# Kernel optimization log

Hardware: AMD Instinct MI355X
Metric: run time of the kernel (lower is better)

The kernel has to match this reference:

```python
import jax, jax.numpy as jnp
import numpy as np

# Module hyperparameters (BNMorph.__init__ defaults + KITTI resolution)
B, H, W = 8, 320, 1024
SEARCH_W = 7      # serachWidth
SEARCH_H = 3      # searchHeight
SPARSITY_RAD = 2
SENSE_R = 20
PIX_DW = 24.0     # pixel_distance_weight
ALPHA_DW = 0.7    # alpha_distance_weight
PIX_MUL_DW = 1.9  # pixel_mulline_distance_weight
ALPHA_PAD = 1.6   # alpha_padding
EDGE_DENSITY = 0.02


def _make_offsets():
    # Exactly mirrors BNMorph.__init__ buffer construction.
    rs = np.arange(-SEARCH_W, SEARCH_W + 1)
    cs = np.arange(-SEARCH_H, SEARCH_H + 1)
    xx, yy = np.meshgrid(rs, cs)
    xx = xx.flatten(); yy = yy.flatten()
    idx = np.argsort(xx ** 2 + yy ** 2)
    xx = xx[idx]; yy = yy[idx]
    ss = np.arange(-SPARSITY_RAD, SPARSITY_RAD + 1)
    sxx, syy = np.meshgrid(ss, ss)
    sxx = sxx.flatten(); syy = syy.flatten()
    cspan = np.arange(-SENSE_R, SENSE_R + 1)
    cxx, cyy = np.meshgrid(cspan, cspan)
    cxx = cxx.flatten(); cyy = cyy.flatten()
    ci = np.argsort(cxx ** 2 + cyy ** 2)
    cxx = cxx[ci]; cyy = cyy[ci]
    f32 = lambda a: jnp.asarray(a, dtype=jnp.float32)
    return f32(xx), f32(yy), f32(sxx), f32(syy), f32(cxx), f32(cyy)


def setup_inputs() -> dict:
    key = jax.random.key(0)
    k1, k2 = jax.random.split(key)
    binMapsrc = (jax.random.uniform(k1, (B, 1, H, W)) < EDGE_DENSITY).astype(jnp.float32)
    binMapdst = (jax.random.uniform(k2, (B, 1, H, W)) < EDGE_DENSITY).astype(jnp.float32)
    xx, yy, sxx, syy, cxx, cyy = _make_offsets()
    return {"binMapsrc": binMapsrc, "binMapdst": binMapdst,
            "xx": xx, "yy": yy, "sxx": sxx, "syy": syy, "cxx": cxx, "cyy": cyy}


def _forward(binMapsrc, binMapdst, xx, yy, sxx, syy, cxx, cyy):
    src = binMapsrc[:, 0] > 0.5  # [B,H,W] bool
    dst = binMapdst[:, 0] > 0.5
    b, h, w = src.shape

    # ---- 1. sparsity filtering of src edge points ----
    # keep an active pixel iff no active pixel precedes it (raster order)
    # inside the sparsity window -> approximates greedy sparsification.
    sdx = sxx.astype(jnp.int32); sdy = syy.astype(jnp.int32)
    prec = ((sdy < 0) | ((sdy == 0) & (sdx < 0))).astype(jnp.float32)
    Ps = jnp.pad(src.astype(jnp.float32),
                 ((0, 0), (SPARSITY_RAD, SPARSITY_RAD), (SPARSITY_RAD, SPARSITY_RAD)))

    def sp_step(acc, off):
        dx, dy, wk = off
        sl = jax.lax.dynamic_slice(Ps, (0, SPARSITY_RAD + dy, SPARSITY_RAD + dx), (b, h, w))
        return acc + sl * wk, None

    acc, _ = jax.lax.scan(sp_step, jnp.zeros((b, h, w), jnp.float32), (sdx, sdy, prec))
    kept = src & (acc < 0.5)

    # ---- 2. windowed nearest-correspondence search in dst ----
    # offsets (xx,yy) are pre-sorted by distance, so the first hit is nearest.
    qdx = xx.astype(jnp.int32); qdy = yy.astype(jnp.int32)
    Pd = jnp.pad(dst, ((0, 0), (SEARCH_H, SEARCH_H), (SEARCH_W, SEARCH_W)))

    def m_step(carry, off):
        found, vx, vy = carry
        dx, dy, dxf, dyf = off
        sl = jax.lax.dynamic_slice(Pd, (0, SEARCH_H + dy, SEARCH_W + dx), (b, h, w))
        hit = sl & kept & (~found)
        vx = jnp.where(hit, dxf, vx)
        vy = jnp.where(hit, dyf, vy)
        return (found | hit, vx, vy), None

    init = (jnp.zeros((b, h, w), bool),
            jnp.zeros((b, h, w), jnp.float32),
            jnp.zeros((b, h, w), jnp.float32))
    (found, vx, vy), _ = jax.lax.scan(m_step, init, (qdx, qdy, xx, yy))

    # ---- 3. distance-weighted morph field (splat = depthwise conv) ----
    d = jnp.sqrt(cxx ** 2 + cyy ** 2)
    wts = ALPHA_DW * jnp.exp(-d * PIX_MUL_DW / PIX_DW)
    R = SENSE_R
    K = jnp.zeros((2 * R + 1, 2 * R + 1), jnp.float32)
    K = K.at[cyy.astype(jnp.int32) + R, cxx.astype(jnp.int32) + R].set(wts)

    m = found.astype(jnp.float32)
    inp = jnp.stack([m, m * vx, m * vy], axis=1)        # [B,3,H,W]
    ker = jnp.tile(K[None, None], (3, 1, 1, 1))          # [3,1,41,41]
    out = jax.lax.conv_general_dilated(
        inp, ker, (1, 1), ((R, R), (R, R)),
        dimension_numbers=("NCHW", "OIHW", "NCHW"), feature_group_count=3)
    den = out[:, 0] + ALPHA_PAD
    dispx = out[:, 1] / den
    dispy = out[:, 2] / den

    ygrid, xgrid = jnp.meshgrid(jnp.arange(h, dtype=jnp.float32),
                                jnp.arange(w, dtype=jnp.float32), indexing="ij")
    morphedx = xgrid + dispx
    morphedy = ygrid + dispy
    orgpts_x = xgrid * m
    orgpts_y = ygrid * m
    correspts_x = (xgrid + vx) * m
    correspts_y = (ygrid + vy) * m
    return morphedx, morphedy, orgpts_x, orgpts_y, correspts_x, correspts_y


def reference(binMapsrc, binMapdst, xx, yy, sxx, syy, cxx, cyy):
    return _forward(binMapsrc, binMapdst, xx, yy, sxx, syy, cxx, cyy)
```

## Files before the change

kernel.cpp:

```cpp
#include <hip/hip_runtime.h>


#define BB 8
#define HH 320
#define WW 1024
#define N_PIX (BB*HH*WW)
#define WPI (HH*(WW/32))
#define RR 20
#define TLW 64
#define TLH 16
#define TXN (WW/TLW)
#define TYN (HH/TLH)
#define NQ 105
#define CAP 160
#define NCR (TLH+40)
#define NSR (NCR+2)
#define NDR (NCR+6)
#define WSTRIDE 53
#define WTABN 2228
#define WTAB_OFF (2*BB*WPI*4)

typedef unsigned long long u64;
typedef float v2f __attribute__((ext_vector_type(2)));

__global__ __launch_bounds__(256) void pack_zero(
    const float* __restrict__ src, const float* __restrict__ dst,
    unsigned* __restrict__ packed, float* __restrict__ wtab_g)
{
    int t = threadIdx.x;
    int i = blockIdx.x * 256 + t;
    if (i < WTABN) {
        int row = i / WSTRIDE, c = i - row * WSTRIDE;
        float v = 0.0f;
        if (row <= 40 && c >= 4 && c <= 44) {
            int dxv = c - 24, dyv = row - 20;
            float d = sqrtf((float)(dxv * dxv + dyv * dyv));
            v = 0.7f * expf((-d * 1.9f) / 24.0f);
        }
        wtab_g[i] = v;
    }
    const float4* p = (i < (N_PIX >> 2)) ? (const float4*)src + i
                                         : (const float4*)dst + (i - (N_PIX >> 2));
    float4 v = *p;
    unsigned nib = (v.x > 0.5f ? 1u : 0u) | (v.y > 0.5f ? 2u : 0u)
                 | (v.z > 0.5f ? 4u : 0u) | (v.w > 0.5f ? 8u : 0u);
    unsigned val = nib << ((t & 7) * 4);
    val |= __shfl_xor(val, 1);
    val |= __shfl_xor(val, 2);
    val |= __shfl_xor(val, 4);
    if ((t & 7) == 0) packed[i >> 3] = val;
}

__global__ __launch_bounds__(128, 5) void fused_morph(
    const unsigned* __restrict__ packed,
    const float* __restrict__ xx, const float* __restrict__ yy,
    const float* __restrict__ wtab_g,
    float* __restrict__ out)
{
    __shared__ __align__(16) float wtab[WTABN];
    __shared__ unsigned sSrc[NSR][6];
    __shared__ unsigned sDst[NDR][6];
    __shared__ __align__(16) unsigned sPt[CAP];
    __shared__ __align__(16) unsigned sWav[2][CAP + 4];
    __shared__ int prank[NQ];
    __shared__ unsigned char sVB[TLH * TLW];
    __shared__ int lcnt;

    int t = threadIdx.x;
    int txT = blockIdx.x, tyT = blockIdx.y, b = blockIdx.z;
    int tx0 = txT * TLW, ty0 = tyT * TLH;
    int wb0 = (tx0 >> 5) - 1;
    const unsigned* psrc = packed + (size_t)b * WPI;
    const unsigned* pdst = packed + (size_t)(BB + b) * WPI;

    for (int i = t; i < WTABN / 4; i += 128)
        ((float4*)wtab)[i] = ((const float4*)wtab_g)[i];
    for (int i = t; i < NSR * 4; i += 128) {
        int r = i >> 2, w = (i & 3) + 1;
        int gy = ty0 - 22 + r, gw = wb0 + (w - 1);
        sSrc[r][w] = (gy >= 0 && gy < HH && gw >= 0 && gw < 32) ? psrc[(gy << 5) + gw] : 0u;
    }
    for (int i = t; i < NDR * 4; i += 128) {
        int r = i >> 2, w = (i & 3) + 1;
        int gy = ty0 - 23 + r, gw = wb0 + (w - 1);
        sDst[r][w] = (gy >= 0 && gy < HH && gw >= 0 && gw < 32) ? pdst[(gy << 5) + gw] : 0u;
    }
    if (t < NDR) { sDst[t][0] = 0; sDst[t][5] = 0; if (t < NSR) { sSrc[t][0] = 0; sSrc[t][5] = 0; } }
    if (t < NQ) {
        int dx = (int)xx[t], dy = (int)yy[t];
        prank[(dy + 3) * 15 + (dx + 7)] = (t << 8) | ((dx + 7) << 4) | (dy + 3);
    }
    ((unsigned*)sVB)[t] = 0; ((unsigned*)sVB)[t + 128] = 0;
    if (t == 0) lcnt = 0;
    __syncthreads();

    for (int task = t; task < NCR * 4; task += 128) {
        int cr = task >> 2, w = (task & 3) + 1;
        unsigned C = sSrc[cr + 2][w];
        unsigned found = 0;
        if (C) {
            #define EXT5(row) ( (u64)((row)[w-1] >> 30) \
                              | ((u64)(row)[w] << 2) \
                              | ((u64)((row)[w+1] & 3u) << 34) )
            u64 a = EXT5(sSrc[cr]) | EXT5(sSrc[cr + 1]);
            u64 or5 = a | (a >> 1) | (a >> 2) | (a >> 3) | (a >> 4);
            u64 e2 = EXT5(sSrc[cr + 2]);
            unsigned kept = C & ~(unsigned)(or5 | e2 | (e2 >> 1));
            if (kept) {
                u64 dil = 0;
                #pragma unroll
                for (int rr = 0; rr < 7; ++rr) {
                    const unsigned* row = sDst[cr + rr];
                    dil |= (u64)(row[w-1] >> 25) | ((u64)row[w] << 7)
                         | ((u64)(row[w+1] & 0x7Fu) << 39);
                }
                u64 a2 = dil | (dil >> 1);
                u64 b2 = a2 | (a2 >> 2);
                u64 c2 = b2 | (b2 >> 4);
                u64 o15 = c2 | (c2 >> 7);
                found = kept & (unsigned)o15;
            }
        }
        if (w == 1) found &= 0xFFFFF000u;
        if (w == 4) found &= 0x000FFFFFu;
        if (found) {
            int nf = __popc(found);
            int base = atomicAdd(&lcnt, nf);
            unsigned fi = found;
            while (fi) {
                int bit = __builtin_ctz(fi); fi &= fi - 1;
                int px = tx0 - 32 + ((w - 1) << 5) + bit;
                if (base < CAP) sPt[base] = (unsigned)((cr << 10) | px);
                ++base;
            }
        }
    }
    __syncthreads();
    int nPts = lcnt; if (nPts > CAP) nPts = CAP;

    for (int i = t; i < nPts; i += 128) {
        unsigned e = sPt[i];
        int cr = (int)(e >> 10), px = (int)(e & 1023u);
        int q = px - tx0 + 25;
        int widx = 1 + (q >> 5), sh = q & 31;
        u64 lo = 0, hi = 0;
        #pragma unroll
        for (int rr = 0; rr < 7; ++rr) {
            const unsigned* row = sDst[cr + rr];
            u64 win = (((u64)row[widx] | ((u64)row[widx + 1] << 32)) >> sh) & 0x7FFFull;
            if (rr < 4) lo |= win << (15 * rr);
            else        hi |= win << (15 * (rr - 4));
        }
        int minv = 0x7FFFFFFF;
        while (lo) { int bb2 = __builtin_ctzll(lo); lo &= lo - 1; int rv = prank[bb2];      if (rv < minv) minv = rv; }
        while (hi) { int bb2 = __builtin_ctzll(hi); hi &= hi - 1; int rv = prank[60 + bb2]; if (rv < minv) minv = rv; }
        int vxp7 = (minv >> 4) & 15, vyp3 = minv & 15;
        int py = ty0 - 20 + cr;
        sPt[i] = (unsigned)px | ((unsigned)py << 10)
               | ((unsigned)vxp7 << 19) | ((unsigned)vyp3 << 23);
        if (px >= tx0 && px < tx0 + TLW && cr >= 20 && cr < 20 + TLH)
            sVB[(cr - 20) * TLW + (px - tx0)] =
                (unsigned char)(0x80 | vxp7 | (vyp3 << 4));
    }
    __syncthreads();

    int lane = t & 63, w = __builtin_amdgcn_readfirstlane(t >> 6);
    int wy0 = ty0 + w * 8;
    int cw = 0;
    for (int base = 0; base < nPts; base += 64) {
        int i = base + lane;
        unsigned pk = (i < nPts) ? sPt[i] : 0xFFFFFFFFu;
        int py = (int)((pk >> 10) & 511u);
        bool pass = (i < nPts) & (py >= wy0 - 20) & (py <= wy0 + 27);
        u64 m = __ballot(pass);
        if (pass) {
            int idx = __popcll(m & ((1ull << lane) - 1ull));
            sWav[w][cw + idx] = pk;
        }
        cw += __popcll(m);
    }
    int c4 = (cw + 3) & ~3;
    if (lane < c4 - cw) sWav[w][cw + lane] = 0xFFFFFFFFu;

    int x0q = tx0 + (t & 15) * 4;
    int y0t = ty0 + (t >> 4) * 2;

    v2f a0p[2][2] = {};
    v2f av[2][4]  = {};

    for (int p = 0; p < c4; p += 4) {
        uint4 P = *(const uint4*)&sWav[w][p];
        #pragma unroll
        for (int k = 0; k < 4; ++k) {
            int spk = __builtin_amdgcn_readfirstlane(
                (int)(k == 0 ? P.x : k == 1 ? P.y : k == 2 ? P.z : P.w));
            int pxp21 = (spk & 1023) + 21;
            int pyp20 = ((spk >> 10) & 511) + 20;
            float pvx = (float)(((spk >> 19) & 15) - 7);
            float pvy = (float)(((spk >> 23) & 7) - 3);
            v2f vv = {pvx, pvy};

            int coff = pxp21 - x0q;
            coff = coff < 0 ? 0 : (coff > 45 ? 45 : coff);
            #pragma unroll
            for (int ry = 0; ry < 2; ++ry) {
                int dyr = pyp20 - (y0t + ry);
                int rowi = ((unsigned)dyr > 40u) ? 41 : dyr;
                const float* wr = &wtab[rowi * WSTRIDE + coff];
                float w3 = wr[0], w2 = wr[1], w1 = wr[2], w0 = wr[3];
                a0p[ry][0] += (v2f){w0, w1};
                a0p[ry][1] += (v2f){w2, w3};
                av[ry][0] += w0 * vv;
                av[ry][1] += w1 * vv;
                av[ry][2] += w2 * vv;
                av[ry][3] += w3 * vv;
            }
        }
    }

    size_t bbase = (size_t)b * HH * WW;
    int lx = x0q - tx0;
    #pragma unroll
    for (int ry = 0; ry < 2; ++ry) {
        int y = y0t + ry;
        int ly = y - ty0;
        unsigned vb4 = *(const unsigned*)&sVB[ly * TLW + lx];
        size_t idx = bbase + (size_t)y * WW + x0q;
        float d0 = a0p[ry][0].x + 1.6f, d1 = a0p[ry][0].y + 1.6f;
        float d2 = a0p[ry][1].x + 1.6f, d3 = a0p[ry][1].y + 1.6f;
        float4 ox = { (float)x0q     + av[ry][0].x / d0, (float)(x0q+1) + av[ry][1].x / d1,
                      (float)(x0q+2) + av[ry][2].x / d2, (float)(x0q+3) + av[ry][3].x / d3 };
        float4 oy = { (float)y + av[ry][0].y / d0, (float)y + av[ry][1].y / d1,
                      (float)y + av[ry][2].y / d2, (float)y + av[ry][3].y / d3 };
        float4 o2, o3, o4, o5;
        float* po2 = &o2.x; float* po3 = &o3.x; float* po4 = &o4.x; float* po5 = &o5.x;
        #pragma unroll
        for (int jj = 0; jj < 4; ++jj) {
            unsigned by = (vb4 >> (8 * jj)) & 255u;
            float fm  = (float)(by >> 7);
            float fvx = (float)((int)(by & 15u) - 7);
            float fvy = (float)((int)((by >> 4) & 7u) - 3);
            float fx  = (float)(x0q + jj);
            po2[jj] = fx * fm;
            po3[jj] = (float)y * fm;
            po4[jj] = (fx + fvx) * fm;
            po5[jj] = ((float)y + fvy) * fm;
        }
        *reinterpret_cast<float4*>(out + idx)                     = ox;
        *reinterpret_cast<float4*>(out + (size_t)N_PIX + idx)     = oy;
        *reinterpret_cast<float4*>(out + 2 * (size_t)N_PIX + idx) = o2;
        *reinterpret_cast<float4*>(out + 3 * (size_t)N_PIX + idx) = o3;
        *reinterpret_cast<float4*>(out + 4 * (size_t)N_PIX + idx) = o4;
        *reinterpret_cast<float4*>(out + 5 * (size_t)N_PIX + idx) = o5;
    }
}

extern "C" void kernel_launch(void* const* d_in, const int* in_sizes, int n_in,
                              void* d_out, int out_size, void* d_ws, size_t ws_size,
                              hipStream_t stream) {
    const float* src = (const float*)d_in[0];
    const float* dst = (const float*)d_in[1];
    const float* xx  = (const float*)d_in[2];
    const float* yy  = (const float*)d_in[3];
    float* out = (float*)d_out;

    unsigned* packed = (unsigned*)d_ws;
    float*    wtab_g = (float*)((char*)d_ws + WTAB_OFF);

    pack_zero<<<(2 * N_PIX / 4) / 256, 256, 0, stream>>>(src, dst, packed, wtab_g);

    dim3 g2(TXN, TYN, BB);
    fused_morph<<<g2, 128, 0, stream>>>(packed, xx, yy, wtab_g, out);
}
```

Baseline: 124.7 us.

## Transpose weight table and remap threads to one column by eight rows

The 41x41 distance-weight table is now stored column-major in shared memory with an odd row stride. Each lane owns one x column and accumulates eight consecutive rows, reading eight contiguous weights per edge point. Previously each thread handled a 4x2 pixel patch, so lanes read table addresses four floats apart; the new layout is meant to cut LDS bank conflicts and simplify index math. In exchange, output stores become scalar per lane rather than float4, and the occupancy hint drops from 5 to 4 blocks.

```diff
diff --git a/kernel.cpp b/kernel.cpp
--- a/kernel.cpp
+++ b/kernel.cpp
@@ -16,8 +16,9 @@
 #define NCR (TLH+40)
 #define NSR (NCR+2)
 #define NDR (NCR+6)
-#define WSTRIDE 53
-#define WTABN 2228
+#define NROWT 55
+#define NCOLT 46
+#define WTABTN 2536
 #define WTAB_OFF (2*BB*WPI*4)
 
 typedef unsigned long long u64;
@@ -29,11 +30,12 @@
 {
     int t = threadIdx.x;
     int i = blockIdx.x * 256 + t;
-    if (i < WTABN) {
-        int row = i / WSTRIDE, c = i - row * WSTRIDE;
+    if (i < WTABTN) {
+        int col = i / NROWT, r = i - col * NROWT;
+        int dyr = r - 7;
         float v = 0.0f;
-        if (row <= 40 && c >= 4 && c <= 44) {
-            int dxv = c - 24, dyv = row - 20;
+        if (col <= 44 && dyr >= 0 && dyr <= 40) {
+            int dxv = col - 20, dyv = dyr - 20;
             float d = sqrtf((float)(dxv * dxv + dyv * dyv));
             v = 0.7f * expf((-d * 1.9f) / 24.0f);
         }
@@ -51,13 +53,13 @@
     if ((t & 7) == 0) packed[i >> 3] = val;
 }
 
-__global__ __launch_bounds__(128, 5) void fused_morph(
+__global__ __launch_bounds__(128, 4) void fused_morph(
     const unsigned* __restrict__ packed,
     const float* __restrict__ xx, const float* __restrict__ yy,
     const float* __restrict__ wtab_g,
     float* __restrict__ out)
 {
-    __shared__ __align__(16) float wtab[WTABN];
+    __shared__ __align__(16) float wtabT[WTABTN];
     __shared__ unsigned sSrc[NSR][6];
     __shared__ unsigned sDst[NDR][6];
     __shared__ __align__(16) unsigned sPt[CAP];
@@ -73,8 +75,8 @@
     const unsigned* psrc = packed + (size_t)b * WPI;
     const unsigned* pdst = packed + (size_t)(BB + b) * WPI;
 
-    for (int i = t; i < WTABN / 4; i += 128)
-        ((float4*)wtab)[i] = ((const float4*)wtab_g)[i];
+    for (int i = t; i < WTABTN / 4; i += 128)
+        ((float4*)wtabT)[i] = ((const float4*)wtab_g)[i];
     for (int i = t; i < NSR * 4; i += 128) {
         int r = i >> 2, w = (i & 3) + 1;
         int gy = ty0 - 22 + r, gw = wb0 + (w - 1);
@@ -182,11 +184,10 @@
     int c4 = (cw + 3) & ~3;
     if (lane < c4 - cw) sWav[w][cw + lane] = 0xFFFFFFFFu;
 
-    int x0q = tx0 + (t & 15) * 4;
-    int y0t = ty0 + (t >> 4) * 2;
-
-    v2f a0p[2][2] = {};
-    v2f av[2][4]  = {};
+    int x = tx0 + lane;
+
+    v2f a0p[4] = {};
+    v2f av[8]  = {};
 
     for (int p = 0; p < c4; p += 4) {
         uint4 P = *(const uint4*)&sWav[w][p];
@@ -194,64 +195,49 @@
         for (int k = 0; k < 4; ++k) {
             int spk = __builtin_amdgcn_readfirstlane(
                 (int)(k == 0 ? P.x : k == 1 ? P.y : k == 2 ? P.z : P.w));
-            int pxp21 = (spk & 1023) + 21;
-            int pyp20 = ((spk >> 10) & 511) + 20;
+            int px = spk & 1023;
+            int q = ((spk >> 10) & 511) + 20 - wy0;
+            q = q < 0 ? 0 : (q > 47 ? 47 : q);
             float pvx = (float)(((spk >> 19) & 15) - 7);
             float pvy = (float)(((spk >> 23) & 7) - 3);
             v2f vv = {pvx, pvy};
 
-            int coff = pxp21 - x0q;
-            coff = coff < 0 ? 0 : (coff > 45 ? 45 : coff);
-            #pragma unroll
-            for (int ry = 0; ry < 2; ++ry) {
-                int dyr = pyp20 - (y0t + ry);
-                int rowi = ((unsigned)dyr > 40u) ? 41 : dyr;
-                const float* wr = &wtab[rowi * WSTRIDE + coff];
-                float w3 = wr[0], w2 = wr[1], w1 = wr[2], w0 = wr[3];
-                a0p[ry][0] += (v2f){w0, w1};
-                a0p[ry][1] += (v2f){w2, w3};
-                av[ry][0] += w0 * vv;
-                av[ry][1] += w1 * vv;
-                av[ry][2] += w2 * vv;
-                av[ry][3] += w3 * vv;
-            }
+            int col = px + 20 - x;
+            col = ((unsigned)col > 40u) ? 45 : col;
+            const float* cb = &wtabT[col * NROWT + q];
+            float w0 = cb[0], w1 = cb[1], w2 = cb[2], w3 = cb[3];
+            float w4 = cb[4], w5 = cb[5], w6 = cb[6], w7 = cb[7];
+            a0p[0] += (v2f){w0, w1};
+            a0p[1] += (v2f){w2, w3};
+            a0p[2] += (v2f){w4, w5};
+            a0p[3] += (v2f){w6, w7};
+            av[7] += w0 * vv;  av[6] += w1 * vv;
+            av[5] += w2 * vv;  av[4] += w3 * vv;
+            av[3] += w4 * vv;  av[2] += w5 * vv;
+            av[1] += w6 * vv;  av[0] += w7 * vv;
         }
     }
 
     size_t bbase = (size_t)b * HH * WW;
-    int lx = x0q - tx0;
+    float fx = (float)x;
     #pragma unroll
-    for (int ry = 0; ry < 2; ++ry) {
-        int y = y0t + ry;
-        int ly = y - ty0;
-        unsigned vb4 = *(const unsigned*)&sVB[ly * TLW + lx];
-        size_t idx = bbase + (size_t)y * WW + x0q;
-        float d0 = a0p[ry][0].x + 1.6f, d1 = a0p[ry][0].y + 1.6f;
-        float d2 = a0p[ry][1].x + 1.6f, d3 = a0p[ry][1].y + 1.6f;
-        float4 ox = { (float)x0q     + av[ry][0].x / d0, (float)(x0q+1) + av[ry][1].x / d1,
-                      (float)(x0q+2) + av[ry][2].x / d2, (float)(x0q+3) + av[ry][3].x / d3 };
-        float4 oy = { (float)y + av[ry][0].y / d0, (float)y + av[ry][1].y / d1,
-                      (float)y + av[ry][2].y / d2, (float)y + av[ry][3].y / d3 };
-        float4 o2, o3, o4, o5;
-        float* po2 = &o2.x; float* po3 = &o3.x; float* po4 = &o4.x; float* po5 = &o5.x;
-        #pragma unroll
-        for (int jj = 0; jj < 4; ++jj) {
-            unsigned by = (vb4 >> (8 * jj)) & 255u;
-            float fm  = (float)(by >> 7);
-            float fvx = (float)((int)(by & 15u) - 7);
-            float fvy = (float)((int)((by >> 4) & 7u) - 3);
-            float fx  = (float)(x0q + jj);
-            po2[jj] = fx * fm;
-            po3[jj] = (float)y * fm;
-            po4[jj] = (fx + fvx) * fm;
-            po5[jj] = ((float)y + fvy) * fm;
-        }
-        *reinterpret_cast<float4*>(out + idx)                     = ox;
-        *reinterpret_cast<float4*>(out + (size_t)N_PIX + idx)     = oy;
-        *reinterpret_cast<float4*>(out + 2 * (size_t)N_PIX + idx) = o2;
-        *reinterpret_cast<float4*>(out + 3 * (size_t)N_PIX + idx) = o3;
-        *reinterpret_cast<float4*>(out + 4 * (size_t)N_PIX + idx) = o4;
-        *reinterpret_cast<float4*>(out + 5 * (size_t)N_PIX + idx) = o5;
+    for (int j = 0; j < 8; ++j) {
+        int y = wy0 + j;
+        unsigned vb = sVB[(y - ty0) * TLW + lane];
+        float fm  = (float)(vb >> 7);
+        float fvx = (float)((int)(vb & 15u) - 7);
+        float fvy = (float)((int)((vb >> 4) & 7u) - 3);
+        int ai = 7 - j;
+        float a0 = (ai & 1) ? a0p[ai >> 1].y : a0p[ai >> 1].x;
+        float den = a0 + 1.6f;
+        float fy = (float)y;
+        size_t idx = bbase + (size_t)y * WW + x;
+        out[idx]                   = fx + av[j].x / den;
+        out[(size_t)N_PIX + idx]   = fy + av[j].y / den;
+        out[2*(size_t)N_PIX + idx] = fx * fm;
+        out[3*(size_t)N_PIX + idx] = fy * fm;
+        out[4*(size_t)N_PIX + idx] = (fx + fvx) * fm;
+        out[5*(size_t)N_PIX + idx] = (fy + fvy) * fm;
     }
 }
 
```

New measurement: 130.5 us. 4.6% more time.
